# Performance work log

Hardware: AMD Instinct MI355X
Metric: run time of the kernel (lower is better)

## Reference

```python
import jax, jax.numpy as jnp
import numpy as np

EMBED_DIM = 512
NUM_JOINTS = 17
HIDDEN = EMBED_DIM * 2  # hidden_ratio=2
B, T = 32, 243


def setup_inputs() -> dict:
    key = jax.random.key(0)
    k_x, k_w1, k_w2 = jax.random.split(key, 3)
    x = jax.random.normal(k_x, (B, T, NUM_JOINTS, EMBED_DIM), dtype=jnp.float32)
    # kaiming_uniform with a=sqrt(5): bound = sqrt(6 / ((1 + a^2) * fan_in)) = sqrt(1/fan_in)
    b1 = float(np.sqrt(1.0 / EMBED_DIM))
    fc1_w = jax.random.uniform(k_w1, (NUM_JOINTS, EMBED_DIM, HIDDEN), minval=-b1, maxval=b1, dtype=jnp.float32)
    fc1_b = jnp.zeros((NUM_JOINTS, HIDDEN), dtype=jnp.float32)
    b2 = float(np.sqrt(1.0 / HIDDEN))
    fc2_w = jax.random.uniform(k_w2, (NUM_JOINTS, HIDDEN, 3), minval=-b2, maxval=b2, dtype=jnp.float32)
    fc2_b = jnp.zeros((NUM_JOINTS, 3), dtype=jnp.float32)
    ln_gamma = jnp.ones((EMBED_DIM,), dtype=jnp.float32)
    ln_beta = jnp.zeros((EMBED_DIM,), dtype=jnp.float32)
    return {"x": x, "ln_gamma": ln_gamma, "ln_beta": ln_beta,
            "fc1_w": fc1_w, "fc1_b": fc1_b, "fc2_w": fc2_w, "fc2_b": fc2_b}


def _layernorm(x, gamma, beta, eps=1e-5):
    mu = jnp.mean(x, axis=-1, keepdims=True)
    var = jnp.mean(jnp.square(x - mu), axis=-1, keepdims=True)
    return (x - mu) * jax.lax.rsqrt(var + eps) * gamma + beta


def reference(x, ln_gamma, ln_beta, fc1_w, fc1_b, fc2_w, fc2_b):
    # x: [B, T, J, d] -> [B, T, J, 3]
    xn = _layernorm(x, ln_gamma, ln_beta)
    h = jnp.einsum('btjd,jdh->btjh', xn, fc1_w) + fc1_b  # [B,T,J,H]
    h = jax.nn.gelu(h, approximate=False)  # torch GELU default is exact (erf)
    y = jnp.einsum('btjh,jho->btjo', h, fc2_w) + fc2_b  # [B,T,J,3]
    return y
```

## Files before the change

kernel.cpp:

```cpp
#include <hip/hip_runtime.h>
#include <hip/hip_bf16.h>

#define JN   17
#define DIM  512
#define HID  1024
#define MTOT 7776
#define MPAD 7808
#define NTHR 512

typedef __attribute__((ext_vector_type(8))) short s16x8;
typedef __attribute__((ext_vector_type(4))) float f32x4;
typedef unsigned short ushort_t;

__device__ __forceinline__ unsigned int f2bf(float f) {
    return (unsigned int)__builtin_bit_cast(unsigned short, __float2bfloat16(f));
}

__device__ __forceinline__ float gelu_erf(float h) {
    float ah = fabsf(h);
    float z  = ah * 0.7071067811865476f;
    float t  = __builtin_amdgcn_rcpf(fmaf(0.3275911f, z, 1.0f));
    float p  = fmaf(fmaf(fmaf(fmaf(1.061405429f, t, -1.453152027f), t,
                              1.421413741f), t, -0.284496736f), t, 0.254829592f);
    float er = 1.0f - p * t * __expf(-z * z);
    return fmaf(0.5f * ah, er, 0.5f * h);
}

__global__ __launch_bounds__(256)
void prep_w1(const float* __restrict__ w1, ushort_t* __restrict__ w1s) {
    int b  = blockIdx.x;
    int nq = b & 3;
    int kc = (b >> 2) & 15;
    int j  = b >> 6;
    int n  = nq * 256 + threadIdx.x;

    const float* src = w1 + ((size_t)j * DIM + kc * 32) * HID + n;
    ushort_t* dst = w1s + (((size_t)j * 16 + kc) * 1024 + n) * 32;

    #pragma unroll
    for (int u = 0; u < 4; ++u) {
        float v[8];
        #pragma unroll
        for (int e = 0; e < 8; ++e) v[e] = src[(u * 8 + e) * HID];
        uint4 qq;
        qq.x = f2bf(v[0]) | (f2bf(v[1]) << 16);
        qq.y = f2bf(v[2]) | (f2bf(v[3]) << 16);
        qq.z = f2bf(v[4]) | (f2bf(v[5]) << 16);
        qq.w = f2bf(v[6]) | (f2bf(v[7]) << 16);
        int p = u ^ ((n >> 1) & 3);
        *(uint4*)(dst + p * 8) = qq;
    }
}

__global__ __launch_bounds__(NTHR)
void prep_xn(const float* __restrict__ x,
             const float* __restrict__ gamma,
             const float* __restrict__ beta,
             ushort_t* __restrict__ xa)
{
    const int lane = threadIdx.x & 63;
    const int wv   = threadIdx.x >> 6;
    const int m    = blockIdx.x * 8 + wv;
    const int j    = blockIdx.y;

    const float4* gp = (const float4*)(gamma + lane * 8);
    const float4* bp = (const float4*)(beta + lane * 8);
    float4 g0 = gp[0], g1 = gp[1];
    float4 e0 = bp[0], e1 = bp[1];

    const float4* xp = (const float4*)(x + ((size_t)m * JN + j) * DIM + lane * 8);
    float4 va = xp[0], vb = xp[1];

    float s  = ((va.x + va.y) + (va.z + va.w)) + ((vb.x + vb.y) + (vb.z + vb.w));
    float s2 = fmaf(va.x, va.x, fmaf(va.y, va.y, fmaf(va.z, va.z, fmaf(va.w, va.w,
               fmaf(vb.x, vb.x, fmaf(vb.y, vb.y, fmaf(vb.z, vb.z, vb.w * vb.w)))))));
    #pragma unroll
    for (int d = 1; d < 64; d <<= 1) {
        s  += __shfl_xor(s,  d);
        s2 += __shfl_xor(s2, d);
    }
    float mu  = s * (1.0f / 512.0f);
    float var = s2 * (1.0f / 512.0f) - mu * mu;
    float rs  = rsqrtf(var + 1e-5f);

    float v0 = fmaf((va.x - mu) * rs, g0.x, e0.x);
    float v1 = fmaf((va.y - mu) * rs, g0.y, e0.y);
    float v2 = fmaf((va.z - mu) * rs, g0.z, e0.z);
    float v3 = fmaf((va.w - mu) * rs, g0.w, e0.w);
    float v4 = fmaf((vb.x - mu) * rs, g1.x, e1.x);
    float v5 = fmaf((vb.y - mu) * rs, g1.y, e1.y);
    float v6 = fmaf((vb.z - mu) * rs, g1.z, e1.z);
    float v7 = fmaf((vb.w - mu) * rs, g1.w, e1.w);
    uint4 qq;
    qq.x = f2bf(v0) | (f2bf(v1) << 16);
    qq.y = f2bf(v2) | (f2bf(v3) << 16);
    qq.z = f2bf(v4) | (f2bf(v5) << 16);
    qq.w = f2bf(v6) | (f2bf(v7) << 16);

    int kc = lane >> 2;
    int p  = (lane & 3) ^ (m & 3) ^ ((m >> 2) & 3);
    *(uint4*)(xa + (((size_t)j * 16 + kc) * MPAD + m) * 32 + p * 8) = qq;
}

#define SMEM_V13 32768
#define NWG13 (61 * 8 * JN)

__global__ __launch_bounds__(256, 3)
void pjh_gemm_v13(const ushort_t* __restrict__ xa,
                  const ushort_t* __restrict__ w1s,
                  const float* __restrict__ b1,
                  const float* __restrict__ w2,
                  float* __restrict__ ypart)
{
    extern __shared__ char smem[];
    const int tid  = threadIdx.x;
    const int lane = tid & 63;
    const int wv   = tid >> 6;
    const int wm   = wv >> 1;
    const int wn   = wv & 1;

    const int xcd  = blockIdx.x & 7;
    const int lid  = blockIdx.x >> 3;
    const int work = xcd * (NWG13 / 8) + lid;
    const int nt2  = work & 7;
    const int rest = work >> 3;
    const int mt   = rest % 61;
    const int j    = rest / 61;

    const char* xaJ = (const char*)xa  + (size_t)j * 16 * MPAD * 64 + (size_t)mt * 8192;
    const char* w1J = (const char*)w1s + (size_t)j * 16 * 65536   + (size_t)nt2 * 8192;
    const size_t xaK = (size_t)MPAD * 64;

    const int g = lane >> 4;
    int aoff[4], boff[4];
    #pragma unroll
    for (int mf = 0; mf < 4; ++mf) {
        int ml = wm * 64 + mf * 16 + (lane & 15);
        int p  = g ^ (ml & 3) ^ ((ml >> 2) & 3);
        aoff[mf] = ml * 64 + p * 16;
    }
    {
        int pB = g ^ (((lane & 15) >> 1) & 3);
        #pragma unroll
        for (int nf = 0; nf < 4; ++nf) {
            int nl = wn * 64 + nf * 16 + (lane & 15);
            int p  = g ^ ((nl >> 1) & 3);
            boff[nf] = 8192 + nl * 64 + p * 16;
        }
        (void)pB;
    }

    const int cT = tid * 16;

#define DMA(SRC, DST) __builtin_amdgcn_global_load_lds(                         \
        (const __attribute__((address_space(1))) unsigned int*)(SRC),           \
        (__attribute__((address_space(3))) unsigned int*)(DST), 16, 0, 0)

#define STAGE(KC, BN) do {                                                      \
        const char* sa = xaJ + (size_t)(KC) * xaK + cT;                         \
        const char* sb = w1J + (size_t)(KC) * 65536 + cT;                       \
        DMA(sa,        smem + (BN) + cT);                                       \
        DMA(sa + 4096, smem + (BN) + 4096 + cT);                                \
        DMA(sb,        smem + (BN) + 8192 + cT);                                \
        DMA(sb + 4096, smem + (BN) + 8192 + 4096 + cT);                         \
    } while (0)

#define STEP(BN) do {                                                           \
        s16x8 aF[4], bF[4];                                                     \
        _Pragma("unroll")                                                       \
        for (int mf = 0; mf < 4; ++mf)                                          \
            aF[mf] = *(const s16x8*)(smem + (BN) + aoff[mf]);                   \
        _Pragma("unroll")                                                       \
        for (int nf = 0; nf < 4; ++nf)                                          \
            bF[nf] = *(const s16x8*)(smem + (BN) + boff[nf]);                   \
        __builtin_amdgcn_s_setprio(1);                                          \
        _Pragma("unroll")                                                       \
        for (int mf = 0; mf < 4; ++mf)                                          \
            _Pragma("unroll")                                                   \
            for (int nf = 0; nf < 4; ++nf)                                      \
                acc[mf][nf] = __builtin_amdgcn_mfma_f32_16x16x32_bf16(aF[mf], bF[nf], acc[mf][nf], 0, 0, 0); \
        __builtin_amdgcn_s_setprio(0);                                          \
    } while (0)

    const f32x4 zero4 = {0.f, 0.f, 0.f, 0.f};
    f32x4 acc[4][4];
    #pragma unroll
    for (int mf = 0; mf < 4; ++mf)
        #pragma unroll
        for (int nf = 0; nf < 4; ++nf) acc[mf][nf] = zero4;

    STAGE(0, 0);
    __syncthreads();

    #pragma unroll 1
    for (int t = 0; t < 16; ++t) {
        int bc = (t & 1) * 16384;
        if (t + 1 < 16) STAGE(t + 1, bc ^ 16384);
        STEP(bc);
        __syncthreads();
    }

    float* Yp = (float*)smem;

    float b1v[4], w20[4], w21[4], w22[4];
    #pragma unroll
    for (int nf = 0; nf < 4; ++nf) {
        int n = nt2 * 128 + wn * 64 + nf * 16 + (lane & 15);
        b1v[nf] = b1[j * HID + n];
        const float* w2p = w2 + ((size_t)j * HID + n) * 3;
        w20[nf] = w2p[0]; w21[nf] = w2p[1]; w22[nf] = w2p[2];
    }

    #pragma unroll
    for (int mf = 0; mf < 4; ++mf) {
        #pragma unroll
        for (int rr = 0; rr < 4; ++rr) {
            float s0 = 0.f, s1 = 0.f, s2 = 0.f;
            #pragma unroll
            for (int nf = 0; nf < 4; ++nf) {
                float gv = gelu_erf(acc[mf][nf][rr] + b1v[nf]);
                s0 = fmaf(gv, w20[nf], s0);
                s1 = fmaf(gv, w21[nf], s1);
                s2 = fmaf(gv, w22[nf], s2);
            }
            s0 += __shfl_xor(s0, 1); s0 += __shfl_xor(s0, 2);
            s0 += __shfl_xor(s0, 4); s0 += __shfl_xor(s0, 8);
            s1 += __shfl_xor(s1, 1); s1 += __shfl_xor(s1, 2);
            s1 += __shfl_xor(s1, 4); s1 += __shfl_xor(s1, 8);
            s2 += __shfl_xor(s2, 1); s2 += __shfl_xor(s2, 2);
            s2 += __shfl_xor(s2, 4); s2 += __shfl_xor(s2, 8);
            if ((lane & 15) == 0) {
                int m = wm * 64 + mf * 16 + (lane >> 4) * 4 + rr;
                Yp[(wn * 128 + m) * 3 + 0] = s0;
                Yp[(wn * 128 + m) * 3 + 1] = s1;
                Yp[(wn * 128 + m) * 3 + 2] = s2;
            }
        }
    }
    __syncthreads();

    for (int idx = tid; idx < 128 * 3; idx += 256) {
        int m = idx / 3;
        int o = idx - m * 3;
        int gr = mt * 128 + m;
        if (gr < MTOT) {
            float v = Yp[m * 3 + o] + Yp[(128 + m) * 3 + o];
            ypart[(((size_t)nt2 * MPAD + gr) * JN + j) * 3 + o] = v;
        }
    }
#undef DMA
#undef STAGE
#undef STEP
}

__global__ __launch_bounds__(512)
void fc2_reduce(const float* __restrict__ ypart,
                const float* __restrict__ b2,
                float* __restrict__ out)
{
    int idx = blockIdx.x * 512 + threadIdx.x;
    if (idx >= MTOT * JN * 3) return;
    int rest = idx / 3;
    int o = idx - rest * 3;
    int j = rest % JN;
    const size_t sl = (size_t)MPAD * JN * 3;
    float v = b2[j * 3 + o];
    #pragma unroll
    for (int s = 0; s < 8; ++s) v += ypart[s * sl + idx];
    out[idx] = v;
}

#define BM3 96
#define A3_OFF 0
#define B3_OFF 98304
#define Y3_OFF 98304
#define SMEM_V3 163840

__global__ __launch_bounds__(NTHR, 2)
void pjh_fused_v3(const float* __restrict__ x,
                  const float* __restrict__ gamma,
                  const float* __restrict__ beta,
                  const ushort_t* __restrict__ w1s,
                  const float* __restrict__ b1,
                  const float* __restrict__ w2,
                  const float* __restrict__ b2,
                  float* __restrict__ out)
{
    extern __shared__ char smem[];
    const int tid  = threadIdx.x;
    const int lane = tid & 63;
    const int wv   = tid >> 6;
    const int wm   = wv >> 2;
    const int wn   = wv & 3;
    const int mt   = blockIdx.x;
    const int j    = blockIdx.y;

    const ushort_t* w1j = w1s + (size_t)j * 16 * 1024 * 32;

    #pragma unroll
    for (int tt = 0; tt < 2; ++tt) {
        const ushort_t* tb = w1j + (size_t)tt * 1024 * 32;
        #pragma unroll
        for (int qq = 0; qq < 2; ++qq) {
            const ushort_t* src = tb + (size_t)(wv * 2 + qq) * 512 + lane * 8;
            void* dst = smem + B3_OFF + tt * 16384 + (wv * 2 + qq) * 1024;
            __builtin_amdgcn_global_load_lds(
                (const __attribute__((address_space(1))) unsigned int*)src,
                (__attribute__((address_space(3))) unsigned int*)dst, 16, 0, 0);
        }
    }

    {
        const float4* gp  = (const float4*)(gamma + lane * 8);
        const float4* bpp = (const float4*)(beta + lane * 8);
        float4 g0 = gp[0], g1 = gp[1];
        float4 e0 = bpp[0], e1 = bpp[1];
        #pragma unroll
        for (int rb = 0; rb < 12; rb += 4) {
            float4 xs[4][2];
            #pragma unroll
            for (int rr = 0; rr < 4; ++rr) {
                int gr = mt * BM3 + wv * 12 + rb + rr;
                const float4* xp = (const float4*)(x + ((size_t)gr * JN + j) * DIM + lane * 8);
                xs[rr][0] = xp[0]; xs[rr][1] = xp[1];
            }
            #pragma unroll
            for (int rr = 0; rr < 4; ++rr) {
                int m = wv * 12 + rb + rr;
                float4 va = xs[rr][0], vb = xs[rr][1];
                float s  = ((va.x + va.y) + (va.z + va.w)) + ((vb.x + vb.y) + (vb.z + vb.w));
                float s2 = fmaf(va.x, va.x, fmaf(va.y, va.y, fmaf(va.z, va.z, fmaf(va.w, va.w,
                           fmaf(vb.x, vb.x, fmaf(vb.y, vb.y, fmaf(vb.z, vb.z, vb.w * vb.w)))))));
                #pragma unroll
                for (int d = 1; d < 64; d <<= 1) {
                    s  += __shfl_xor(s,  d);
                    s2 += __shfl_xor(s2, d);
                }
                float mu  = s * (1.0f / 512.0f);
                float var = s2 * (1.0f / 512.0f) - mu * mu;
                float rs  = rsqrtf(var + 1e-5f);
                float v0 = fmaf((va.x - mu) * rs, g0.x, e0.x);
                float v1 = fmaf((va.y - mu) * rs, g0.y, e0.y);
                float v2 = fmaf((va.z - mu) * rs, g0.z, e0.z);
                float v3 = fmaf((va.w - mu) * rs, g0.w, e0.w);
                float v4 = fmaf((vb.x - mu) * rs, g1.x, e1.x);
                float v5 = fmaf((vb.y - mu) * rs, g1.y, e1.y);
                float v6 = fmaf((vb.z - mu) * rs, g1.z, e1.z);
                float v7 = fmaf((vb.w - mu) * rs, g1.w, e1.w);
                uint4 qq;
                qq.x = f2bf(v0) | (f2bf(v1) << 16);
                qq.y = f2bf(v2) | (f2bf(v3) << 16);
                qq.z = f2bf(v4) | (f2bf(v5) << 16);
                qq.w = f2bf(v6) | (f2bf(v7) << 16);
                *(uint4*)(smem + A3_OFF + m * 1024 + ((lane ^ (m & 7)) * 16)) = qq;
            }
        }
    }

    __syncthreads();

    float yr[3][4][3];
    #pragma unroll
    for (int a = 0; a < 3; ++a)
        #pragma unroll
        for (int rr = 0; rr < 4; ++rr)
            #pragma unroll
            for (int o = 0; o < 3; ++o) yr[a][rr][o] = 0.f;

    const f32x4 zero4 = {0.f, 0.f, 0.f, 0.f};
    f32x4 acc[3][4];
    #pragma unroll
    for (int mf = 0; mf < 3; ++mf)
        #pragma unroll
        for (int nf = 0; nf < 4; ++nf) acc[mf][nf] = zero4;

    #pragma unroll 1
    for (int t = 0; t < 64; ++t) {
        if (t + 2 < 64) {
            int kc = (t + 2) & 15, nt = (t + 2) >> 4;
            const ushort_t* tb = w1j + ((size_t)kc * 1024 + nt * 256) * 32;
            int bb = ((t + 2) & 3) * 16384;
            #pragma unroll
            for (int qq = 0; qq < 2; ++qq) {
                const ushort_t* src = tb + (size_t)(wv * 2 + qq) * 512 + lane * 8;
                void* dst = smem + B3_OFF + bb + (wv * 2 + qq) * 1024;
                __builtin_amdgcn_global_load_lds(
                    (const __attribute__((address_space(1))) unsigned int*)src,
                    (__attribute__((address_space(3))) unsigned int*)dst, 16, 0, 0);
            }
        }

        int kc = t & 15;
        int bb = (t & 3) * 16384;
        int g  = lane >> 4;
        s16x8 aF[3], bF[4];
        #pragma unroll
        for (int mf = 0; mf < 3; ++mf) {
            int m  = wm * 48 + mf * 16 + (lane & 15);
            int ul = kc * 4 + g;
            aF[mf] = *(const s16x8*)(smem + A3_OFF + m * 1024 + ((ul ^ (m & 7)) * 16));
        }
        #pragma unroll
        for (int nf = 0; nf < 4; ++nf) {
            int nl = wn * 64 + nf * 16 + (lane & 15);
            int p  = g ^ ((nl >> 1) & 3);
            bF[nf] = *(const s16x8*)(smem + B3_OFF + bb + (nl * 4 + p) * 16);
        }

        __builtin_amdgcn_s_setprio(1);
        #pragma unroll
        for (int mf = 0; mf < 3; ++mf)
            #pragma unroll
            for (int nf = 0; nf < 4; ++nf)
                acc[mf][nf] = __builtin_amdgcn_mfma_f32_16x16x32_bf16(aF[mf], bF[nf], acc[mf][nf], 0, 0, 0);
        __builtin_amdgcn_s_setprio(0);

        if ((t & 15) == 15) {
            int nt = t >> 4;
            #pragma unroll
            for (int nf = 0; nf < 4; ++nf) {
                int n = nt * 256 + wn * 64 + nf * 16 + (lane & 15);
                float b1v = b1[j * HID + n];
                const float* w2p = w2 + ((size_t)j * HID + n) * 3;
                float w20 = w2p[0], w21 = w2p[1], w22 = w2p[2];
                #pragma unroll
                for (int mf = 0; mf < 3; ++mf) {
                    #pragma unroll
                    for (int rr = 0; rr < 4; ++rr) {
                        float gv = gelu_erf(acc[mf][nf][rr] + b1v);
                        yr[mf][rr][0] = fmaf(gv, w20, yr[mf][rr][0]);
                        yr[mf][rr][1] = fmaf(gv, w21, yr[mf][rr][1]);
                        yr[mf][rr][2] = fmaf(gv, w22, yr[mf][rr][2]);
                    }
                }
            }
            #pragma unroll
            for (int mf = 0; mf < 3; ++mf)
                #pragma unroll
                for (int nf = 0; nf < 4; ++nf)
                    acc[mf][nf] = zero4;
        }

        if (t < 62) {
            asm volatile("s_waitcnt vmcnt(2)" ::: "memory");
        } else {
            asm volatile("s_waitcnt vmcnt(0)" ::: "memory");
        }
        __builtin_amdgcn_s_barrier();
    }

    #pragma unroll
    for (int mf = 0; mf < 3; ++mf)
        #pragma unroll
        for (int rr = 0; rr < 4; ++rr)
            #pragma unroll
            for (int o = 0; o < 3; ++o) {
                float v = yr[mf][rr][o];
                v += __shfl_xor(v, 1);
                v += __shfl_xor(v, 2);
                v += __shfl_xor(v, 4);
                v += __shfl_xor(v, 8);
                yr[mf][rr][o] = v;
            }

    __syncthreads();

    float* Yp = (float*)(smem + Y3_OFF);
    if ((lane & 15) == 0) {
        int mrow = lane >> 4;
        #pragma unroll
        for (int mf = 0; mf < 3; ++mf)
            #pragma unroll
            for (int rr = 0; rr < 4; ++rr) {
                int m = wm * 48 + mf * 16 + mrow * 4 + rr;
                #pragma unroll
                for (int o = 0; o < 3; ++o)
                    Yp[(wn * BM3 + m) * 3 + o] = yr[mf][rr][o];
            }
    }
    __syncthreads();

    if (tid < BM3 * 3) {
        int m = tid / 3;
        int o = tid - m * 3;
        int gr = mt * BM3 + m;
        float v = Yp[m * 3 + o] + Yp[(BM3 + m) * 3 + o]
                + Yp[(2 * BM3 + m) * 3 + o] + Yp[(3 * BM3 + m) * 3 + o]
                + b2[j * 3 + o];
        out[((size_t)gr * JN + j) * 3 + o] = v;
    }
}

extern "C" void kernel_launch(void* const* d_in, const int* in_sizes, int n_in,
                              void* d_out, int out_size, void* d_ws, size_t ws_size,
                              hipStream_t stream) {
    (void)in_sizes; (void)n_in; (void)out_size;
    const float* x   = (const float*)d_in[0];
    const float* ga  = (const float*)d_in[1];
    const float* be  = (const float*)d_in[2];
    const float* w1  = (const float*)d_in[3];
    const float* b1  = (const float*)d_in[4];
    const float* w2  = (const float*)d_in[5];
    const float* b2  = (const float*)d_in[6];
    float* out = (float*)d_out;

    const size_t xa_bytes  = (size_t)JN * 16 * MPAD * 32 * sizeof(ushort_t);
    const size_t w1s_bytes = (size_t)JN * 16 * 1024 * 32 * sizeof(ushort_t);
    const size_t yp_bytes  = (size_t)8 * MPAD * JN * 3 * sizeof(float);

    if (ws_size >= xa_bytes + w1s_bytes + yp_bytes) {
        ushort_t* xa  = (ushort_t*)d_ws;
        ushort_t* w1s = (ushort_t*)((char*)d_ws + xa_bytes);
        float* ypart  = (float*)((char*)d_ws + xa_bytes + w1s_bytes);
        prep_xn<<<dim3(MTOT / 8, JN), NTHR, 0, stream>>>(x, ga, be, xa);
        prep_w1<<<JN * 16 * 4, 256, 0, stream>>>(w1, w1s);
        hipFuncSetAttribute((const void*)pjh_gemm_v13,
                            hipFuncAttributeMaxDynamicSharedMemorySize, SMEM_V13);
        pjh_gemm_v13<<<NWG13, 256, SMEM_V13, stream>>>(xa, w1s, b1, w2, ypart);
        fc2_reduce<<<(MTOT * JN * 3 + 511) / 512, 512, 0, stream>>>(ypart, b2, out);
    } else {
        ushort_t* w1s = (ushort_t*)d_ws;
        prep_w1<<<JN * 16 * 4, 256, 0, stream>>>(w1, w1s);
        hipFuncSetAttribute((const void*)pjh_fused_v3,
                            hipFuncAttributeMaxDynamicSharedMemorySize, SMEM_V3);
        dim3 grid(MTOT / BM3, JN);
        pjh_fused_v3<<<grid, NTHR, SMEM_V3, stream>>>(x, ga, be, w1s, b1, w2, b2, out);
    }
}
```

Before: 310.3 us.

## Load W1 fragments directly from global into registers, stage only A in LDS

The GEMM kernel no longer stages the W1 tile through LDS. Each wave loads its B fragments straight from global memory into registers, double-buffered two K-steps ahead. Only the activation tile goes through LDS, which halves shared memory per block from 32KB to 16KB. This cuts LDS traffic and footprint but adds redundant global/L2 reads of W1 across the two wm waves, and may raise register pressure.

```diff
diff --git a/kernel.cpp b/kernel.cpp
--- a/kernel.cpp
+++ b/kernel.cpp
@@ -102,11 +102,11 @@
     *(uint4*)(xa + (((size_t)j * 16 + kc) * MPAD + m) * 32 + p * 8) = qq;
 }
 
-#define SMEM_V13 32768
-#define NWG13 (61 * 8 * JN)
+#define SMEM_V15 16384
+#define NWG15 (61 * 8 * JN)
 
 __global__ __launch_bounds__(256, 3)
-void pjh_gemm_v13(const ushort_t* __restrict__ xa,
+void pjh_gemm_v15(const ushort_t* __restrict__ xa,
                   const ushort_t* __restrict__ w1s,
                   const float* __restrict__ b1,
                   const float* __restrict__ w2,
@@ -121,34 +121,27 @@
 
     const int xcd  = blockIdx.x & 7;
     const int lid  = blockIdx.x >> 3;
-    const int work = xcd * (NWG13 / 8) + lid;
+    const int work = xcd * (NWG15 / 8) + lid;
     const int nt2  = work & 7;
     const int rest = work >> 3;
     const int mt   = rest % 61;
     const int j    = rest / 61;
 
-    const char* xaJ = (const char*)xa  + (size_t)j * 16 * MPAD * 64 + (size_t)mt * 8192;
-    const char* w1J = (const char*)w1s + (size_t)j * 16 * 65536   + (size_t)nt2 * 8192;
+    const char* xaJ = (const char*)xa + (size_t)j * 16 * MPAD * 64 + (size_t)mt * 8192;
     const size_t xaK = (size_t)MPAD * 64;
 
     const int g = lane >> 4;
-    int aoff[4], boff[4];
+    const int pB = g ^ (((lane & 15) >> 1) & 3);
+    const ushort_t* bB0 = w1s + (size_t)j * 16 * 1024 * 32
+                              + ((size_t)nt2 * 128 + wn * 64 + (lane & 15)) * 32 + pB * 8;
+
+    int aoff[4];
     #pragma unroll
     for (int mf = 0; mf < 4; ++mf) {
         int ml = wm * 64 + mf * 16 + (lane & 15);
         int p  = g ^ (ml & 3) ^ ((ml >> 2) & 3);
         aoff[mf] = ml * 64 + p * 16;
     }
-    {
-        int pB = g ^ (((lane & 15) >> 1) & 3);
-        #pragma unroll
-        for (int nf = 0; nf < 4; ++nf) {
-            int nl = wn * 64 + nf * 16 + (lane & 15);
-            int p  = g ^ ((nl >> 1) & 3);
-            boff[nf] = 8192 + nl * 64 + p * 16;
-        }
-        (void)pB;
-    }
 
     const int cT = tid * 16;
 
@@ -156,29 +149,29 @@
         (const __attribute__((address_space(1))) unsigned int*)(SRC),           \
         (__attribute__((address_space(3))) unsigned int*)(DST), 16, 0, 0)
 
-#define STAGE(KC, BN) do {                                                      \
+#define STAGE_A(KC, BN) do {                                                    \
         const char* sa = xaJ + (size_t)(KC) * xaK + cT;                         \
-        const char* sb = w1J + (size_t)(KC) * 65536 + cT;                       \
         DMA(sa,        smem + (BN) + cT);                                       \
         DMA(sa + 4096, smem + (BN) + 4096 + cT);                                \
-        DMA(sb,        smem + (BN) + 8192 + cT);                                \
-        DMA(sb + 4096, smem + (BN) + 8192 + 4096 + cT);                         \
     } while (0)
 
-#define STEP(BN) do {                                                           \
-        s16x8 aF[4], bF[4];                                                     \
+#define LOADB(FB, KC) do {                                                      \
+        const ushort_t* bp_ = bB0 + (size_t)(KC) * 32768;                       \
+        _Pragma("unroll")                                                       \
+        for (int nf = 0; nf < 4; ++nf) FB[nf] = *(const s16x8*)(bp_ + nf * 512);\
+    } while (0)
+
+#define STEP(BN, FB) do {                                                       \
+        s16x8 aF[4];                                                            \
         _Pragma("unroll")                                                       \
         for (int mf = 0; mf < 4; ++mf)                                          \
             aF[mf] = *(const s16x8*)(smem + (BN) + aoff[mf]);                   \
-        _Pragma("unroll")                                                       \
-        for (int nf = 0; nf < 4; ++nf)                                          \
-            bF[nf] = *(const s16x8*)(smem + (BN) + boff[nf]);                   \
         __builtin_amdgcn_s_setprio(1);                                          \
         _Pragma("unroll")                                                       \
         for (int mf = 0; mf < 4; ++mf)                                          \
             _Pragma("unroll")                                                   \
             for (int nf = 0; nf < 4; ++nf)                                      \
-                acc[mf][nf] = __builtin_amdgcn_mfma_f32_16x16x32_bf16(aF[mf], bF[nf], acc[mf][nf], 0, 0, 0); \
+                acc[mf][nf] = __builtin_amdgcn_mfma_f32_16x16x32_bf16(aF[mf], FB[nf], acc[mf][nf], 0, 0, 0); \
         __builtin_amdgcn_s_setprio(0);                                          \
     } while (0)
 
@@ -189,14 +182,23 @@
         #pragma unroll
         for (int nf = 0; nf < 4; ++nf) acc[mf][nf] = zero4;
 
-    STAGE(0, 0);
+    s16x8 fB0[4], fB1[4];
+
+    STAGE_A(0, 0);
+    LOADB(fB0, 0);
+    LOADB(fB1, 1);
     __syncthreads();
 
     #pragma unroll 1
-    for (int t = 0; t < 16; ++t) {
-        int bc = (t & 1) * 16384;
-        if (t + 1 < 16) STAGE(t + 1, bc ^ 16384);
-        STEP(bc);
+    for (int tp = 0; tp < 8; ++tp) {
+        if (2 * tp + 1 < 16) STAGE_A(2 * tp + 1, 8192);
+        STEP(0, fB0);
+        if (2 * tp + 2 < 16) LOADB(fB0, 2 * tp + 2);
+        __syncthreads();
+
+        if (2 * tp + 2 < 16) STAGE_A(2 * tp + 2, 0);
+        STEP(8192, fB1);
+        if (2 * tp + 3 < 16) LOADB(fB1, 2 * tp + 3);
         __syncthreads();
     }
 
@@ -249,7 +251,8 @@
         }
     }
 #undef DMA
-#undef STAGE
+#undef STAGE_A
+#undef LOADB
 #undef STEP
 }
 
@@ -514,9 +517,9 @@
         float* ypart  = (float*)((char*)d_ws + xa_bytes + w1s_bytes);
         prep_xn<<<dim3(MTOT / 8, JN), NTHR, 0, stream>>>(x, ga, be, xa);
         prep_w1<<<JN * 16 * 4, 256, 0, stream>>>(w1, w1s);
-        hipFuncSetAttribute((const void*)pjh_gemm_v13,
-                            hipFuncAttributeMaxDynamicSharedMemorySize, SMEM_V13);
-        pjh_gemm_v13<<<NWG13, 256, SMEM_V13, stream>>>(xa, w1s, b1, w2, ypart);
+        hipFuncSetAttribute((const void*)pjh_gemm_v15,
+                            hipFuncAttributeMaxDynamicSharedMemorySize, SMEM_V15);
+        pjh_gemm_v15<<<NWG15, 256, SMEM_V15, stream>>>(xa, w1s, b1, w2, ypart);
         fc2_reduce<<<(MTOT * JN * 3 + 511) / 512, 512, 0, stream>>>(ypart, b2, out);
     } else {
         ushort_t* w1s = (ushort_t*)d_ws;
```

Result: slower. 343.6 us (+10.7%).
